# Kernel tuning notes

Hardware: AMD Instinct MI355X
Metric: run time of the kernel (lower is better)

## Reference

```python
import jax, jax.numpy as jnp
import numpy as np

LAMBDA_WEIGHT = 1.0


def _soft_argmax(logits):
    # differentiable_argmax: sum_c softmax(logits)[c] * c along class dim
    nc = logits.shape[1]
    probs = jax.nn.softmax(logits, axis=1)
    idx = jnp.arange(nc, dtype=logits.dtype)[None, :, None, None]
    return jnp.sum(probs * idx, axis=1)  # [B, H, W]


def _pair_loss(mask, d):
    # mask: [L] bool over row-major flattened HxW; d: [L] float (col - row).
    # torch.where returns row-major order, coord[:,1]-coord[:,0] == d at masked
    # pixels; second diff is |d_i - d_prev| over consecutive masked pixels.
    L = mask.shape[0]
    pos = jnp.where(mask, jnp.arange(L), -1)
    last = jax.lax.cummax(pos, axis=0)                 # last masked index <= i
    prev = jnp.concatenate([jnp.full((1,), -1), last[:-1]])  # strictly before i
    valid = mask & (prev >= 0)
    dprev = d[jnp.clip(prev, 0, L - 1)]
    s = jnp.sum(jnp.where(valid, jnp.abs(d - dprev), 0.0))
    npairs = jnp.sum(valid)
    npts = jnp.sum(mask)
    mean = s / jnp.maximum(npairs, 1).astype(d.dtype)
    # N==0 contributes 0 (the `continue`); N==1 gives an empty-mean (NaN) in
    # torch -- guarded to 0 here (such degenerate classes are skipped).
    return jnp.where(npts >= 2, mean / (npts + 1).astype(d.dtype), 0.0)


def reference(logits, labels):
    bs, nc, h, w = logits.shape
    seg = jnp.floor(jax.lax.stop_gradient(_soft_argmax(logits))).astype(jnp.int32)
    seg = seg.reshape(bs, h * w)                       # [B, L] row-major
    # d[i] = col - row for flattened index i
    i = jnp.arange(h * w)
    d = ((i % w) - (i // w)).astype(jnp.float32)       # [L]
    classes = jnp.arange(1, nc, dtype=jnp.int32)       # skip background c=0
    masks = seg[:, None, :] == classes[None, :, None]  # [B, nc-1, L]
    per = jax.vmap(jax.vmap(_pair_loss, in_axes=(0, None)), in_axes=(0, None))(masks, d)
    return jnp.sum(per) * LAMBDA_WEIGHT


def setup_inputs() -> dict:
    key = jax.random.key(0)
    k1, k2 = jax.random.split(key)
    logits = jax.random.normal(k1, (16, 7, 368, 640), dtype=jnp.float32)
    labels = jax.random.randint(k2, (16, 368, 640), 0, 7, dtype=jnp.int64)
    return {"logits": logits, "labels": labels}
```

## Files before the change

### kernel.cpp

```cpp
#include <hip/hip_runtime.h>
#include <cstdint>
#include <cstddef>

#define BB 16
#define CC 7
#define HH 368
#define WW 640
#define LL (HH * WW)
#define NCLS 6
#define NCOMBO (BB * NCLS)
#define PAIRS_PB (HH / 2)
#define NPAIRS (BB * PAIRS_PB)
#define NBLK (NPAIRS / 4)

typedef float v4f __attribute__((ext_vector_type(4)));

__device__ inline v4f ntload4(const float* p) {
    return __builtin_nontemporal_load(reinterpret_cast<const v4f*>(p));
}

__global__ __launch_bounds__(256) void rowstat_kernel(const float* __restrict__ logits,
                                                      int4* __restrict__ rowStats) {
    int t     = threadIdx.x;
    int w     = t >> 6;
    int lane  = t & 63;
    int grow2 = blockIdx.x * 4 + w;
    int b  = grow2 / PAIRS_PB;
    int r0 = (grow2 - b * PAIRS_PB) * 2;
    const float* pairbase = logits + (size_t)b * CC * LL + (size_t)r0 * WW;

    float sacc[20], wacc[20];
#pragma unroll
    for (int k = 0; k < 20; ++k) { sacc[k] = 0.0f; wacc[k] = 0.0f; }

#pragma unroll
    for (int c = 0; c < CC; ++c) {
        const float* p = pairbase + (size_t)c * LL;
        v4f v[5];
#pragma unroll
        for (int it = 0; it < 5; ++it)
            v[it] = ntload4(p + it * 256 + lane * 4);
        float fc = (float)c;
#pragma unroll
        for (int it = 0; it < 5; ++it) {
            float e0 = __expf(v[it].x), e1 = __expf(v[it].y);
            float e2 = __expf(v[it].z), e3 = __expf(v[it].w);
            sacc[it * 4 + 0] += e0; wacc[it * 4 + 0] += e0 * fc;
            sacc[it * 4 + 1] += e1; wacc[it * 4 + 1] += e1 * fc;
            sacc[it * 4 + 2] += e2; wacc[it * 4 + 2] += e2 * fc;
            sacc[it * 4 + 3] += e3; wacc[it * 4 + 3] += e3 * fc;
        }
    }

    int cnt[NCLS][2], mn[NCLS][2], mx[NCLS][2];
#pragma unroll
    for (int c = 0; c < NCLS; ++c)
#pragma unroll
        for (int R = 0; R < 2; ++R) { cnt[c][R] = 0; mn[c][R] = 1 << 30; mx[c][R] = -1; }

#pragma unroll
    for (int it = 0; it < 5; ++it) {
#pragma unroll
        for (int k = 0; k < 4; ++k) {
            int idx = it * 4 + k;
            int sv  = (int)floorf(__fdividef(wacc[idx], sacc[idx]));
            int px  = it * 256 + lane * 4 + k;
            if (it < 2) {
                int col = px;
#pragma unroll
                for (int c = 0; c < NCLS; ++c) {
                    int m = (sv == c + 1);
                    cnt[c][0] += m;
                    mn[c][0] = m ? min(mn[c][0], col) : mn[c][0];
                    mx[c][0] = m ? max(mx[c][0], col) : mx[c][0];
                }
            } else if (it > 2) {
                int col = px - WW;
#pragma unroll
                for (int c = 0; c < NCLS; ++c) {
                    int m = (sv == c + 1);
                    cnt[c][1] += m;
                    mn[c][1] = m ? min(mn[c][1], col) : mn[c][1];
                    mx[c][1] = m ? max(mx[c][1], col) : mx[c][1];
                }
            } else {
                int pr  = px >= WW;
                int col = pr ? (px - WW) : px;
#pragma unroll
                for (int c = 0; c < NCLS; ++c) {
                    int m  = (sv == c + 1);
                    int m0 = m & (pr == 0), m1 = m & pr;
                    cnt[c][0] += m0;
                    mn[c][0] = m0 ? min(mn[c][0], col) : mn[c][0];
                    mx[c][0] = m0 ? max(mx[c][0], col) : mx[c][0];
                    cnt[c][1] += m1;
                    mn[c][1] = m1 ? min(mn[c][1], col) : mn[c][1];
                    mx[c][1] = m1 ? max(mx[c][1], col) : mx[c][1];
                }
            }
        }
    }

#pragma unroll
    for (int c = 0; c < NCLS; ++c) {
#pragma unroll
        for (int R = 0; R < 2; ++R) {
            if (__ballot(cnt[c][R] > 0) == 0ull) { cnt[c][R] = 0; continue; }
#pragma unroll
            for (int off = 1; off < 64; off <<= 1) {
                cnt[c][R] += __shfl_down(cnt[c][R], off, 64);
                mn[c][R]  = min(mn[c][R], __shfl_down(mn[c][R], off, 64));
                mx[c][R]  = max(mx[c][R], __shfl_down(mx[c][R], off, 64));
            }
        }
    }

    if (lane == 0) {
#pragma unroll
        for (int c = 0; c < NCLS; ++c)
#pragma unroll
            for (int R = 0; R < 2; ++R)
                rowStats[(size_t)(b * NCLS + c) * HH + r0 + R] =
                    make_int4(cnt[c][R], mn[c][R], mx[c][R], 0);
    }
}

struct St { int S, cnt, first, last; };

__device__ inline St comb(const St& a, const St& b) {
    St r;
    int both = (a.cnt > 0) & (b.cnt > 0);
    r.S     = a.S + b.S + (both ? abs(b.first - a.last) : 0);
    r.cnt   = a.cnt + b.cnt;
    r.first = (a.cnt > 0) ? a.first : b.first;
    r.last  = (b.cnt > 0) ? b.last : a.last;
    return r;
}

__device__ inline St shfl_down_st(const St& s, int off) {
    St r;
    r.S     = __shfl_down(s.S, off, 64);
    r.cnt   = __shfl_down(s.cnt, off, 64);
    r.first = __shfl_down(s.first, off, 64);
    r.last  = __shfl_down(s.last, off, 64);
    return r;
}

__global__ __launch_bounds__(256) void combine_kernel(const int4* __restrict__ rowStats,
                                                      float* __restrict__ out) {
    int combo = blockIdx.x;
    int t = threadIdx.x;
    const int4* rp = rowStats + (size_t)combo * HH;

    St st{0, 0, 0, 0};
    if (t < HH / 2) {
#pragma unroll
        for (int q = 0; q < 2; ++q) {
            int row = 2 * t + q;
            int4 v = rp[row];
            if (v.x > 0) {
                St rs{v.z - v.y, v.x, v.y - row, v.z - row};
                st = comb(st, rs);
            }
        }
    }

#pragma unroll
    for (int off = 1; off < 64; off <<= 1) {
        St o = shfl_down_st(st, off);
        st = comb(st, o);
    }

    __shared__ int4 ws[4];
    int wave = t >> 6;
    if ((t & 63) == 0) ws[wave] = make_int4(st.S, st.cnt, st.first, st.last);
    __syncthreads();

    if (t == 0) {
        St acc{ws[0].x, ws[0].y, ws[0].z, ws[0].w};
#pragma unroll
        for (int q = 1; q < 4; ++q) {
            St o{ws[q].x, ws[q].y, ws[q].z, ws[q].w};
            acc = comb(acc, o);
        }
        int n = acc.cnt;
        if (n >= 2) {
            double res = ((double)acc.S / (double)(n - 1)) / (double)(n + 1);
            atomicAdd(out, (float)res);
        }
    }
}

extern "C" void kernel_launch(void* const* d_in, const int* in_sizes, int n_in,
                              void* d_out, int out_size, void* d_ws, size_t ws_size,
                              hipStream_t stream) {
    const float* logits = (const float*)d_in[0];
    float* out = (float*)d_out;

    int4* rowStats = (int4*)d_ws;

    hipMemsetAsync(out, 0, sizeof(float) * out_size, stream);
    rowstat_kernel<<<NBLK, 256, 0, stream>>>(logits, rowStats);
    combine_kernel<<<NCOMBO, 256, 0, stream>>>(rowStats, out);
}
```

Measured before the change: 160.7 us.

## Prefetch next class channel, pre-combine row pairs, drop memset, one combo per wave

The row-stat kernel now double-buffers the logits loads, issuing the next class channel's five vector loads before doing the exp work on the current one, so memory latency is hidden within each wave. It also folds the two rows of each pair into one combined segment record, which halves the intermediate data. The separate memset launch is replaced by block 0 zeroing the output inside the first kernel. The combine kernel now maps one combo per wave with no shared-memory or syncthreads step. The costs are more registers held by the prefetch buffers, and correctness now relies on the first kernel finishing before the second kernel's atomics touch the output.

```diff
diff --git a/kernel.cpp b/kernel.cpp
--- a/kernel.cpp
+++ b/kernel.cpp
@@ -19,37 +19,74 @@
     return __builtin_nontemporal_load(reinterpret_cast<const v4f*>(p));
 }
 
+struct St { int S, cnt, first, last; };
+
+__device__ inline St comb(const St& a, const St& b) {
+    St r;
+    int both = (a.cnt > 0) & (b.cnt > 0);
+    r.S     = a.S + b.S + (both ? abs(b.first - a.last) : 0);
+    r.cnt   = a.cnt + b.cnt;
+    r.first = (a.cnt > 0) ? a.first : b.first;
+    r.last  = (b.cnt > 0) ? b.last : a.last;
+    return r;
+}
+
+__device__ inline St shfl_down_st(const St& s, int off) {
+    St r;
+    r.S     = __shfl_down(s.S, off, 64);
+    r.cnt   = __shfl_down(s.cnt, off, 64);
+    r.first = __shfl_down(s.first, off, 64);
+    r.last  = __shfl_down(s.last, off, 64);
+    return r;
+}
+
 __global__ __launch_bounds__(256) void rowstat_kernel(const float* __restrict__ logits,
-                                                      int4* __restrict__ rowStats) {
+                                                      int4* __restrict__ pairStats,
+                                                      float* __restrict__ out,
+                                                      int out_n) {
+    if (blockIdx.x == 0 && threadIdx.x == 0) {
+        int n = out_n < 4 ? out_n : 4;
+        for (int i = 0; i < n; ++i) out[i] = 0.0f;
+    }
+
     int t     = threadIdx.x;
     int w     = t >> 6;
     int lane  = t & 63;
     int grow2 = blockIdx.x * 4 + w;
     int b  = grow2 / PAIRS_PB;
-    int r0 = (grow2 - b * PAIRS_PB) * 2;
+    int pidx = grow2 - b * PAIRS_PB;
+    int r0 = pidx * 2;
     const float* pairbase = logits + (size_t)b * CC * LL + (size_t)r0 * WW;
 
     float sacc[20], wacc[20];
 #pragma unroll
     for (int k = 0; k < 20; ++k) { sacc[k] = 0.0f; wacc[k] = 0.0f; }
 
+    v4f va[5], vb[5];
+#pragma unroll
+    for (int it = 0; it < 5; ++it)
+        va[it] = ntload4(pairbase + it * 256 + lane * 4);
+
 #pragma unroll
     for (int c = 0; c < CC; ++c) {
-        const float* p = pairbase + (size_t)c * LL;
-        v4f v[5];
-#pragma unroll
-        for (int it = 0; it < 5; ++it)
-            v[it] = ntload4(p + it * 256 + lane * 4);
+        if (c + 1 < CC) {
+            const float* pn = pairbase + (size_t)(c + 1) * LL;
+#pragma unroll
+            for (int it = 0; it < 5; ++it)
+                vb[it] = ntload4(pn + it * 256 + lane * 4);
+        }
         float fc = (float)c;
 #pragma unroll
         for (int it = 0; it < 5; ++it) {
-            float e0 = __expf(v[it].x), e1 = __expf(v[it].y);
-            float e2 = __expf(v[it].z), e3 = __expf(v[it].w);
+            float e0 = __expf(va[it].x), e1 = __expf(va[it].y);
+            float e2 = __expf(va[it].z), e3 = __expf(va[it].w);
             sacc[it * 4 + 0] += e0; wacc[it * 4 + 0] += e0 * fc;
             sacc[it * 4 + 1] += e1; wacc[it * 4 + 1] += e1 * fc;
             sacc[it * 4 + 2] += e2; wacc[it * 4 + 2] += e2 * fc;
             sacc[it * 4 + 3] += e3; wacc[it * 4 + 3] += e3 * fc;
         }
+#pragma unroll
+        for (int it = 0; it < 5; ++it) va[it] = vb[it];
     }
 
     int cnt[NCLS][2], mn[NCLS][2], mx[NCLS][2];
@@ -117,49 +154,40 @@
 
     if (lane == 0) {
 #pragma unroll
-        for (int c = 0; c < NCLS; ++c)
-#pragma unroll
-            for (int R = 0; R < 2; ++R)
-                rowStats[(size_t)(b * NCLS + c) * HH + r0 + R] =
-                    make_int4(cnt[c][R], mn[c][R], mx[c][R], 0);
-    }
-}
-
-struct St { int S, cnt, first, last; };
-
-__device__ inline St comb(const St& a, const St& b) {
-    St r;
-    int both = (a.cnt > 0) & (b.cnt > 0);
-    r.S     = a.S + b.S + (both ? abs(b.first - a.last) : 0);
-    r.cnt   = a.cnt + b.cnt;
-    r.first = (a.cnt > 0) ? a.first : b.first;
-    r.last  = (b.cnt > 0) ? b.last : a.last;
-    return r;
-}
-
-__device__ inline St shfl_down_st(const St& s, int off) {
-    St r;
-    r.S     = __shfl_down(s.S, off, 64);
-    r.cnt   = __shfl_down(s.cnt, off, 64);
-    r.first = __shfl_down(s.first, off, 64);
-    r.last  = __shfl_down(s.last, off, 64);
-    return r;
-}
-
-__global__ __launch_bounds__(256) void combine_kernel(const int4* __restrict__ rowStats,
+        for (int c = 0; c < NCLS; ++c) {
+            St pa{0, 0, 0, 0};
+            if (cnt[c][0] > 0) {
+                pa.S = mx[c][0] - mn[c][0]; pa.cnt = cnt[c][0];
+                pa.first = mn[c][0] - r0;   pa.last = mx[c][0] - r0;
+            }
+            if (cnt[c][1] > 0) {
+                St pb;
+                pb.S = mx[c][1] - mn[c][1]; pb.cnt = cnt[c][1];
+                pb.first = mn[c][1] - (r0 + 1); pb.last = mx[c][1] - (r0 + 1);
+                pa = comb(pa, pb);
+            }
+            pairStats[(size_t)(b * NCLS + c) * PAIRS_PB + pidx] =
+                make_int4(pa.S, pa.cnt, pa.first, pa.last);
+        }
+    }
+}
+
+__global__ __launch_bounds__(256) void combine_kernel(const int4* __restrict__ pairStats,
                                                       float* __restrict__ out) {
-    int combo = blockIdx.x;
-    int t = threadIdx.x;
-    const int4* rp = rowStats + (size_t)combo * HH;
+    int t    = threadIdx.x;
+    int wave = t >> 6;
+    int lane = t & 63;
+    int combo = blockIdx.x * 4 + wave;
+    const int4* rp = pairStats + (size_t)combo * PAIRS_PB;
 
     St st{0, 0, 0, 0};
-    if (t < HH / 2) {
-#pragma unroll
-        for (int q = 0; q < 2; ++q) {
-            int row = 2 * t + q;
-            int4 v = rp[row];
-            if (v.x > 0) {
-                St rs{v.z - v.y, v.x, v.y - row, v.z - row};
+#pragma unroll
+    for (int q = 0; q < 3; ++q) {
+        int idx = lane * 3 + q;
+        if (idx < PAIRS_PB) {
+            int4 v = rp[idx];
+            if (v.y > 0) {
+                St rs{v.x, v.y, v.z, v.w};
                 st = comb(st, rs);
             }
         }
@@ -171,21 +199,10 @@
         st = comb(st, o);
     }
 
-    __shared__ int4 ws[4];
-    int wave = t >> 6;
-    if ((t & 63) == 0) ws[wave] = make_int4(st.S, st.cnt, st.first, st.last);
-    __syncthreads();
-
-    if (t == 0) {
-        St acc{ws[0].x, ws[0].y, ws[0].z, ws[0].w};
-#pragma unroll
-        for (int q = 1; q < 4; ++q) {
-            St o{ws[q].x, ws[q].y, ws[q].z, ws[q].w};
-            acc = comb(acc, o);
-        }
-        int n = acc.cnt;
+    if (lane == 0) {
+        int n = st.cnt;
         if (n >= 2) {
-            double res = ((double)acc.S / (double)(n - 1)) / (double)(n + 1);
+            double res = ((double)st.S / (double)(n - 1)) / (double)(n + 1);
             atomicAdd(out, (float)res);
         }
     }
@@ -197,9 +214,8 @@
     const float* logits = (const float*)d_in[0];
     float* out = (float*)d_out;
 
-    int4* rowStats = (int4*)d_ws;
-
-    hipMemsetAsync(out, 0, sizeof(float) * out_size, stream);
-    rowstat_kernel<<<NBLK, 256, 0, stream>>>(logits, rowStats);
-    combine_kernel<<<NCOMBO, 256, 0, stream>>>(rowStats, out);
-}
+    int4* pairStats = (int4*)d_ws;
+
+    rowstat_kernel<<<NBLK, 256, 0, stream>>>(logits, pairStats, out, out_size);
+    combine_kernel<<<NCOMBO / 4, 256, 0, stream>>>(pairStats, out);
+}
```

After: 160.3 us. No clear change (-0.2%).
